# Performance work log

Measured on AMD Instinct MI355X. Metric: run time of the kernel, lower is better.

Reference implementation:

```python
import jax, jax.numpy as jnp
import numpy as np
from jax import lax

KS = 11          # kernel_size
SIGMA = 1.5
MAX_VAL = 1.0
C1 = (0.01 * MAX_VAL) ** 2
C2 = (0.03 * MAX_VAL) ** 2
EPS = 1e-12
PAD = KS // 2    # use_padding=True -> reflect pad


def _gaussian_kernel3d():
    ax = jnp.arange(KS, dtype=jnp.float32) - (KS - 1) / 2.0
    g = jnp.exp(-(ax[:, None, None] ** 2 + ax[None, :, None] ** 2 + ax[None, None, :] ** 2)
                / (2.0 * SIGMA ** 2))
    return g / g.sum()  # (KS, KS, KS)


def setup_inputs() -> dict:
    key = jax.random.key(0)
    k1, k2 = jax.random.split(key)
    shape = (2, 1, 160, 160, 160)
    source = jax.random.uniform(k1, shape, dtype=jnp.float32)
    reference_vol = jax.random.uniform(k2, shape, dtype=jnp.float32)
    return {"source": source, "reference": reference_vol}


def reference(source, reference):
    B, C, H, W, D = source.shape
    # reflect pad spatial dims (torch 'reflect' == numpy 'reflect')
    pad_cfg = ((0, 0), (0, 0), (PAD, PAD), (PAD, PAD), (PAD, PAD))
    src = jnp.pad(source, pad_cfg, mode="reflect")
    ref = jnp.pad(reference, pad_cfg, mode="reflect")

    # fuse the 5 depthwise convolutions into one grouped conv over stacked channels
    stacked = jnp.concatenate([src, ref, src * src, ref * ref, src * ref], axis=1)  # (B,5C,...)
    kern = _gaussian_kernel3d()[None, None]                      # (1,1,KS,KS,KS)
    kern = jnp.tile(kern, (5 * C, 1, 1, 1, 1))                   # (5C,1,KS,KS,KS)
    out = lax.conv_general_dilated(
        stacked, kern, window_strides=(1, 1, 1), padding="VALID",
        feature_group_count=5 * C,
        dimension_numbers=("NCDHW", "OIDHW", "NCDHW"))           # (B,5C,H,W,D)

    mu1 = out[:, 0 * C:1 * C]
    mu2 = out[:, 1 * C:2 * C]
    m11 = out[:, 2 * C:3 * C]
    m22 = out[:, 3 * C:4 * C]
    m12 = out[:, 4 * C:5 * C]

    mu1_sq = mu1 * mu1
    mu2_sq = mu2 * mu2
    mu1_mu2 = mu1 * mu2
    sigma1_sq = m11 - mu1_sq
    sigma2_sq = m22 - mu2_sq
    sigma12 = m12 - mu1_mu2

    numerator = (2.0 * mu1_mu2 + C1) * (2.0 * sigma12 + C2)
    denominator = (mu1_sq + mu2_sq + C1) * (sigma1_sq + sigma2_sq + C2)
    ssim = numerator / (denominator + EPS)
    return 1.0 - ssim.mean()
```

## Files before the change

### kernel.cpp

```cpp
#include <hip/hip_runtime.h>
#include <math.h>

#define HH 160
#define WW 160
#define DD 160
#define VOL (HH*WW*DD)
#define KS 11
#define PAD 5
#define NBATCH 2
#define NTOT (NBATCH*VOL)

#define WT 16
#define DT 16
#define HT 32
#define WPN (WT + 2*PAD)
#define NSTEP (HT + 2*PAD)
#define RS 68
#define P01S 36
#define P4S 17

typedef float v2f __attribute__((ext_vector_type(2)));
typedef float v4f __attribute__((ext_vector_type(4)));

struct Wts { float w[KS]; };

__device__ __forceinline__ int mirror(int i, int n) {
    if (i < 0) i = -i;
    if (i >= n) i = 2*n - 2 - i;
    return i;
}

__device__ __forceinline__ v2f pk_fma(v2f a, v2f b, v2f c) {
    v2f d;
    asm("v_pk_fma_f32 %0, %1, %2, %3" : "=v"(d) : "v"(a), "v"(b), "v"(c));
    return d;
}
__device__ __forceinline__ v2f pk_mul(v2f a, v2f b) {
    v2f d;
    asm("v_pk_mul_f32 %0, %1, %2" : "=v"(d) : "v"(a), "v"(b));
    return d;
}

__global__ void init_out(float* out) {
    if (threadIdx.x == 0 && blockIdx.x == 0) out[0] = 1.0f;
}

__global__ __launch_bounds__(256) void fused(const float* __restrict__ src,
                                             const float* __restrict__ ref,
                                             float* __restrict__ out,
                                             Wts wts, float scale) {
    __shared__ float raw[WPN * RS];
    __shared__ float pl01[WPN * P01S];
    __shared__ float pl23[WPN * P01S];
    __shared__ float pl4 [WPN * P4S];

    const int bx  = blockIdx.x;
    const int dt_ = bx % (DD/DT);
    const int wt_ = (bx / (DD/DT)) % (WW/WT);
    const int ht_ = (bx / ((DD/DT)*(WW/WT))) % (HH/HT);
    const int b   = bx / ((DD/DT)*(WW/WT)*(HH/HT));
    const int d0 = dt_*DT, w0 = wt_*WT, h0 = ht_*HT;

    const int  dbase = (d0 == 0) ? 0 : ((d0 == DD-DT) ? DD-32 : d0-8);
    const bool dedge = (d0 == 0) || (d0 == DD-DT);

    const int tid = threadIdx.x;
    const float* __restrict__ sp = src + (size_t)b*VOL;
    const float* __restrict__ rp = ref + (size_t)b*VOL;

    const bool sact = (tid < WPN*8);
    const int  swp = tid >> 3, sq = tid & 7;
    const int  sgoff  = mirror(w0 - PAD + (sact ? swp : 0), WW)*DD + dbase + sq*4;
    const int  srawof = swp*RS + sq*8;

    const int  p_dl  = tid & 15;
    const int  p_wp0 = tid >> 4;
    const bool p_act1 = (tid < WPN*DT - 256);
    const int  pw0_01 = p_wp0*P01S + 2*p_dl;
    const int  pw0_4  = p_wp0*P4S  + p_dl;
    const int  pw1_01 = (p_wp0+16)*P01S + 2*p_dl;
    const int  pw1_4  = (p_wp0+16)*P4S  + p_dl;

    const int wl = tid >> 4, dl2 = tid & 15;

    v2f wpk[KS];
#pragma unroll
    for (int k = 0; k < KS; ++k) { wpk[k].x = wts.w[k]; wpk[k].y = wts.w[k]; }

    v2f acc01[KS], acc23[KS];
    float acc4[KS];
#pragma unroll
    for (int s = 0; s < KS; ++s) {
        acc01[s] = (v2f)0.f; acc23[s] = (v2f)0.f; acc4[s] = 0.f;
    }

    float ssum = 0.f;

    v4f ra = (v4f)0.f, rb_ = (v4f)0.f;
    {
        const int hm = mirror(h0 - PAD, HH);
        if (sact) {
            const float* g = sp + (size_t)hm*(WW*DD) + sgoff;
            const float* h = rp + (size_t)hm*(WW*DD) + sgoff;
            ra  = *reinterpret_cast<const v4f*>(g);
            rb_ = *reinterpret_cast<const v4f*>(h);
        }
    }

    for (int tb = 0; tb < 44; tb += 11) {
#pragma unroll
        for (int ts = 0; ts < 11; ++ts) {
            const int t = tb + ts;
            if (t < NSTEP) {
                if (sact) {
                    v4f c0, c1;
                    c0.x = ra.x; c0.y = rb_.x; c0.z = ra.y; c0.w = rb_.y;
                    c1.x = ra.z; c1.y = rb_.z; c1.z = ra.w; c1.w = rb_.w;
                    *reinterpret_cast<v4f*>(&raw[srawof])     = c0;
                    *reinterpret_cast<v4f*>(&raw[srawof + 4]) = c1;
                }
                __syncthreads();

                {
                    v2f mu_a = (v2f)0.f, mm_a = (v2f)0.f;
                    v2f mu_b = (v2f)0.f, mm_b = (v2f)0.f;
                    float m12a = 0.f, m12b = 0.f;
                    if (!dedge) {
                        const float* r0 = &raw[p_wp0*RS + 2*(p_dl + 3)];
                        const float* r1 = r0 + 16*RS;
#pragma unroll
                        for (int k = 0; k < KS; ++k) {
                            v2f w  = wpk[k];
                            v2f sr = *reinterpret_cast<const v2f*>(r0 + 2*k);
                            mu_a = pk_fma(sr, w, mu_a);
                            mm_a = pk_fma(pk_mul(sr, sr), w, mm_a);
                            m12a = fmaf(w.x, sr.x*sr.y, m12a);
                        }
                        if (p_act1) {
#pragma unroll
                            for (int k = 0; k < KS; ++k) {
                                v2f w  = wpk[k];
                                v2f sr = *reinterpret_cast<const v2f*>(r1 + 2*k);
                                mu_b = pk_fma(sr, w, mu_b);
                                mm_b = pk_fma(pk_mul(sr, sr), w, mm_b);
                                m12b = fmaf(w.x, sr.x*sr.y, m12b);
                            }
                        }
                    } else {
#pragma unroll
                        for (int k = 0; k < KS; ++k) {
                            const int widx = mirror(d0 + p_dl - PAD + k, DD) - dbase;
                            v2f w  = wpk[k];
                            v2f sr = *reinterpret_cast<const v2f*>(&raw[p_wp0*RS + 2*widx]);
                            mu_a = pk_fma(sr, w, mu_a);
                            mm_a = pk_fma(pk_mul(sr, sr), w, mm_a);
                            m12a = fmaf(w.x, sr.x*sr.y, m12a);
                            if (p_act1) {
                                v2f sr2 = *reinterpret_cast<const v2f*>(&raw[(p_wp0+16)*RS + 2*widx]);
                                mu_b = pk_fma(sr2, w, mu_b);
                                mm_b = pk_fma(pk_mul(sr2, sr2), w, mm_b);
                                m12b = fmaf(w.x, sr2.x*sr2.y, m12b);
                            }
                        }
                    }
                    *reinterpret_cast<v2f*>(&pl01[pw0_01]) = mu_a;
                    *reinterpret_cast<v2f*>(&pl23[pw0_01]) = mm_a;
                    pl4[pw0_4] = m12a;
                    if (p_act1) {
                        *reinterpret_cast<v2f*>(&pl01[pw1_01]) = mu_b;
                        *reinterpret_cast<v2f*>(&pl23[pw1_01]) = mm_b;
                        pl4[pw1_4] = m12b;
                    }
                }

                {
                    const int tn = t + 1;
                    if (sact && tn < NSTEP) {
                        const int hm = mirror(h0 - PAD + tn, HH);
                        const float* g = sp + (size_t)hm*(WW*DD) + sgoff;
                        const float* h = rp + (size_t)hm*(WW*DD) + sgoff;
                        ra  = *reinterpret_cast<const v4f*>(g);
                        rb_ = *reinterpret_cast<const v4f*>(h);
                    }
                }
                __syncthreads();

                {
                    v2f v01 = (v2f)0.f, v23 = (v2f)0.f;
                    float v4v = 0.f;
                    const float* q01 = &pl01[wl*P01S + 2*dl2];
                    const float* q23 = &pl23[wl*P01S + 2*dl2];
                    const float* q4  = &pl4 [wl*P4S  + dl2];
#pragma unroll
                    for (int k = 0; k < KS; ++k) {
                        v2f w = wpk[k];
                        v01 = pk_fma(*reinterpret_cast<const v2f*>(q01 + k*P01S), w, v01);
                        v23 = pk_fma(*reinterpret_cast<const v2f*>(q23 + k*P01S), w, v23);
                        v4v = fmaf(w.x, q4[k*P4S], v4v);
                    }
#pragma unroll
                    for (int m = 0; m < 11; ++m) {
                        const int slot = (ts + m) % 11;
                        v2f wt = wpk[10 - m];
                        acc01[slot] = pk_fma(v01, wt, acc01[slot]);
                        acc23[slot] = pk_fma(v23, wt, acc23[slot]);
                        acc4[slot]  = fmaf(wt.x, v4v, acc4[slot]);
                    }
                    if (t >= 10) {
                        float mu1 = acc01[ts].x, mu2 = acc01[ts].y;
                        float m11 = acc23[ts].x, m22 = acc23[ts].y, m12 = acc4[ts];
                        float mu1sq = mu1*mu1, mu2sq = mu2*mu2, mu12 = mu1*mu2;
                        float s1 = m11 - mu1sq, s2 = m22 - mu2sq, s12 = m12 - mu12;
                        const float C1 = 1e-4f, C2 = 9e-4f;
                        float num = (2.f*mu12 + C1) * (2.f*s12 + C2);
                        float den = (mu1sq + mu2sq + C1) * (s1 + s2 + C2);
                        ssum += num / (den + 1e-12f);
                    }
                    acc01[ts] = (v2f)0.f; acc23[ts] = (v2f)0.f; acc4[ts] = 0.f;
                }
            }
        }
    }

#pragma unroll
    for (int off = 32; off > 0; off >>= 1)
        ssum += __shfl_down(ssum, off, 64);
    __shared__ float lsum[4];
    int lane = tid & 63, wid = tid >> 6;
    if (lane == 0) lsum[wid] = ssum;
    __syncthreads();
    if (tid == 0)
        atomicAdd(out, -(lsum[0]+lsum[1]+lsum[2]+lsum[3]) * scale);
}

extern "C" void kernel_launch(void* const* d_in, const int* in_sizes, int n_in,
                              void* d_out, int out_size, void* d_ws, size_t ws_size,
                              hipStream_t stream) {
    const float* src = (const float*)d_in[0];
    const float* ref = (const float*)d_in[1];
    float* out = (float*)d_out;

    Wts wts;
    {
        double g[KS], s = 0.0;
        for (int i = 0; i < KS; ++i) {
            double a = (double)i - (KS - 1) / 2.0;
            g[i] = exp(-(a * a) / (2.0 * 1.5 * 1.5));
            s += g[i];
        }
        for (int i = 0; i < KS; ++i) wts.w[i] = (float)(g[i] / s);
    }

    const float scale = 1.0f / (float)NTOT;

    init_out<<<1, 64, 0, stream>>>(out);
    const int g = NBATCH * (HH/HT) * (WW/WT) * (DD/DT);
    fused<<<g, 256, 0, stream>>>(src, ref, out, wts, scale);
}
```

Baseline: 213.0 us.

## Double-buffer LDS stages to drop a barrier and prefetch two rows ahead

Double-buffers the raw and pass-1 LDS arrays so each H-step needs one __syncthreads instead of two. Global loads are issued two rows ahead, and the raw tile is preloaded before the loop. The change also refactors the D-pass to compute w*x once and reuse it for the sum, square and cross terms. It precomputes the mirrored edge offsets, replaces the division with rcp plus one Newton step, and changes the P4S padding. The cost is doubled LDS use, which can lower occupancy, and possible bank conflicts from the changed P4S stride.

Result: no change. 212.5 us (-0.2%).

```diff
diff --git a/kernel.cpp b/kernel.cpp
--- a/kernel.cpp
+++ b/kernel.cpp
@@ -17,7 +17,10 @@
 #define NSTEP (HT + 2*PAD)
 #define RS 68
 #define P01S 36
-#define P4S 17
+#define P4S 16
+#define RAW_W (WPN*RS)
+#define P01_W (WPN*P01S)
+#define P4_W  (WPN*P4S)
 
 typedef float v2f __attribute__((ext_vector_type(2)));
 typedef float v4f __attribute__((ext_vector_type(4)));
@@ -31,14 +34,13 @@
 }
 
 __device__ __forceinline__ v2f pk_fma(v2f a, v2f b, v2f c) {
-    v2f d;
-    asm("v_pk_fma_f32 %0, %1, %2, %3" : "=v"(d) : "v"(a), "v"(b), "v"(c));
-    return d;
+    v2f d; asm("v_pk_fma_f32 %0, %1, %2, %3" : "=v"(d) : "v"(a), "v"(b), "v"(c)); return d;
 }
 __device__ __forceinline__ v2f pk_mul(v2f a, v2f b) {
-    v2f d;
-    asm("v_pk_mul_f32 %0, %1, %2" : "=v"(d) : "v"(a), "v"(b));
-    return d;
+    v2f d; asm("v_pk_mul_f32 %0, %1, %2" : "=v"(d) : "v"(a), "v"(b)); return d;
+}
+__device__ __forceinline__ v2f pk_add(v2f a, v2f b) {
+    v2f d; asm("v_pk_add_f32 %0, %1, %2" : "=v"(d) : "v"(a), "v"(b)); return d;
 }
 
 __global__ void init_out(float* out) {
@@ -49,10 +51,10 @@
                                              const float* __restrict__ ref,
                                              float* __restrict__ out,
                                              Wts wts, float scale) {
-    __shared__ float raw[WPN * RS];
-    __shared__ float pl01[WPN * P01S];
-    __shared__ float pl23[WPN * P01S];
-    __shared__ float pl4 [WPN * P4S];
+    __shared__ float raw [2*RAW_W];
+    __shared__ float pl01[2*P01_W];
+    __shared__ float pl23[2*P01_W];
+    __shared__ float pl4 [2*P4_W];
 
     const int bx  = blockIdx.x;
     const int dt_ = bx % (DD/DT);
@@ -81,6 +83,13 @@
     const int  pw1_01 = (p_wp0+16)*P01S + 2*p_dl;
     const int  pw1_4  = (p_wp0+16)*P4S  + p_dl;
 
+    int eoff[KS];
+    if (dedge) {
+#pragma unroll
+        for (int k = 0; k < KS; ++k)
+            eoff[k] = 2*(mirror(d0 + p_dl - PAD + k, DD) - dbase);
+    }
+
     const int wl = tid >> 4, dl2 = tid & 15;
 
     v2f wpk[KS];
@@ -94,18 +103,24 @@
         acc01[s] = (v2f)0.f; acc23[s] = (v2f)0.f; acc4[s] = 0.f;
     }
 
+    v4f ra = (v4f)0.f, rb_ = (v4f)0.f;
+    if (sact) {
+        const size_t o0 = (size_t)mirror(h0 - PAD, HH)*(WW*DD) + sgoff;
+        ra  = *reinterpret_cast<const v4f*>(sp + o0);
+        rb_ = *reinterpret_cast<const v4f*>(rp + o0);
+        v4f c0, c1;
+        c0.x=ra.x; c0.y=rb_.x; c0.z=ra.y; c0.w=rb_.y;
+        c1.x=ra.z; c1.y=rb_.z; c1.z=ra.w; c1.w=rb_.w;
+        *reinterpret_cast<v4f*>(&raw[srawof])     = c0;
+        *reinterpret_cast<v4f*>(&raw[srawof + 4]) = c1;
+        const size_t o1 = (size_t)mirror(h0 - PAD + 1, HH)*(WW*DD) + sgoff;
+        ra  = *reinterpret_cast<const v4f*>(sp + o1);
+        rb_ = *reinterpret_cast<const v4f*>(rp + o1);
+    }
+    __syncthreads();
+
     float ssum = 0.f;
-
-    v4f ra = (v4f)0.f, rb_ = (v4f)0.f;
-    {
-        const int hm = mirror(h0 - PAD, HH);
-        if (sact) {
-            const float* g = sp + (size_t)hm*(WW*DD) + sgoff;
-            const float* h = rp + (size_t)hm*(WW*DD) + sgoff;
-            ra  = *reinterpret_cast<const v4f*>(g);
-            rb_ = *reinterpret_cast<const v4f*>(h);
-        }
-    }
+    int rawRd = 0, rawWr = RAW_W, po01 = 0, po4 = 0;
 
     for (int tb = 0; tb < 44; tb += 11) {
 #pragma unroll
@@ -114,83 +129,74 @@
             if (t < NSTEP) {
                 if (sact) {
                     v4f c0, c1;
-                    c0.x = ra.x; c0.y = rb_.x; c0.z = ra.y; c0.w = rb_.y;
-                    c1.x = ra.z; c1.y = rb_.z; c1.z = ra.w; c1.w = rb_.w;
-                    *reinterpret_cast<v4f*>(&raw[srawof])     = c0;
-                    *reinterpret_cast<v4f*>(&raw[srawof + 4]) = c1;
-                }
-                __syncthreads();
-
-                {
-                    v2f mu_a = (v2f)0.f, mm_a = (v2f)0.f;
-                    v2f mu_b = (v2f)0.f, mm_b = (v2f)0.f;
-                    float m12a = 0.f, m12b = 0.f;
-                    if (!dedge) {
-                        const float* r0 = &raw[p_wp0*RS + 2*(p_dl + 3)];
-                        const float* r1 = r0 + 16*RS;
+                    c0.x=ra.x; c0.y=rb_.x; c0.z=ra.y; c0.w=rb_.y;
+                    c1.x=ra.z; c1.y=rb_.z; c1.z=ra.w; c1.w=rb_.w;
+                    *reinterpret_cast<v4f*>(&raw[rawWr + srawof])     = c0;
+                    *reinterpret_cast<v4f*>(&raw[rawWr + srawof + 4]) = c1;
+                    const size_t on = (size_t)mirror(h0 - PAD + t + 2, HH)*(WW*DD) + sgoff;
+                    ra  = *reinterpret_cast<const v4f*>(sp + on);
+                    rb_ = *reinterpret_cast<const v4f*>(rp + on);
+                }
+
+                v2f mu_a=(v2f)0.f, mm_a=(v2f)0.f, mu_b=(v2f)0.f, mm_b=(v2f)0.f;
+                float m12a=0.f, m12b=0.f;
+                if (!dedge) {
+                    const float* r0 = &raw[rawRd + p_wp0*RS + 2*p_dl + 6];
+                    const float* r1 = r0 + 16*RS;
+#pragma unroll
+                    for (int k = 0; k < KS; ++k) {
+                        v2f sr = *reinterpret_cast<const v2f*>(r0 + 2*k);
+                        v2f p  = pk_mul(sr, wpk[k]);
+                        mu_a = pk_add(mu_a, p);
+                        mm_a = pk_fma(p, sr, mm_a);
+                        m12a = fmaf(p.x, sr.y, m12a);
+                    }
+                    if (p_act1) {
 #pragma unroll
                         for (int k = 0; k < KS; ++k) {
-                            v2f w  = wpk[k];
-                            v2f sr = *reinterpret_cast<const v2f*>(r0 + 2*k);
-                            mu_a = pk_fma(sr, w, mu_a);
-                            mm_a = pk_fma(pk_mul(sr, sr), w, mm_a);
-                            m12a = fmaf(w.x, sr.x*sr.y, m12a);
+                            v2f sr = *reinterpret_cast<const v2f*>(r1 + 2*k);
+                            v2f p  = pk_mul(sr, wpk[k]);
+                            mu_b = pk_add(mu_b, p);
+                            mm_b = pk_fma(p, sr, mm_b);
+                            m12b = fmaf(p.x, sr.y, m12b);
                         }
+                    }
+                } else {
+                    const float* rb0 = &raw[rawRd + p_wp0*RS];
+                    const float* rb1 = rb0 + 16*RS;
+#pragma unroll
+                    for (int k = 0; k < KS; ++k) {
+                        v2f sr = *reinterpret_cast<const v2f*>(rb0 + eoff[k]);
+                        v2f p  = pk_mul(sr, wpk[k]);
+                        mu_a = pk_add(mu_a, p);
+                        mm_a = pk_fma(p, sr, mm_a);
+                        m12a = fmaf(p.x, sr.y, m12a);
                         if (p_act1) {
-#pragma unroll
-                            for (int k = 0; k < KS; ++k) {
-                                v2f w  = wpk[k];
-                                v2f sr = *reinterpret_cast<const v2f*>(r1 + 2*k);
-                                mu_b = pk_fma(sr, w, mu_b);
-                                mm_b = pk_fma(pk_mul(sr, sr), w, mm_b);
-                                m12b = fmaf(w.x, sr.x*sr.y, m12b);
-                            }
+                            v2f sr2 = *reinterpret_cast<const v2f*>(rb1 + eoff[k]);
+                            v2f p2  = pk_mul(sr2, wpk[k]);
+                            mu_b = pk_add(mu_b, p2);
+                            mm_b = pk_fma(p2, sr2, mm_b);
+                            m12b = fmaf(p2.x, sr2.y, m12b);
                         }
-                    } else {
-#pragma unroll
-                        for (int k = 0; k < KS; ++k) {
-                            const int widx = mirror(d0 + p_dl - PAD + k, DD) - dbase;
-                            v2f w  = wpk[k];
-                            v2f sr = *reinterpret_cast<const v2f*>(&raw[p_wp0*RS + 2*widx]);
-                            mu_a = pk_fma(sr, w, mu_a);
-                            mm_a = pk_fma(pk_mul(sr, sr), w, mm_a);
-                            m12a = fmaf(w.x, sr.x*sr.y, m12a);
-                            if (p_act1) {
-                                v2f sr2 = *reinterpret_cast<const v2f*>(&raw[(p_wp0+16)*RS + 2*widx]);
-                                mu_b = pk_fma(sr2, w, mu_b);
-                                mm_b = pk_fma(pk_mul(sr2, sr2), w, mm_b);
-                                m12b = fmaf(w.x, sr2.x*sr2.y, m12b);
-                            }
-                        }
-                    }
-                    *reinterpret_cast<v2f*>(&pl01[pw0_01]) = mu_a;
-                    *reinterpret_cast<v2f*>(&pl23[pw0_01]) = mm_a;
-                    pl4[pw0_4] = m12a;
-                    if (p_act1) {
-                        *reinterpret_cast<v2f*>(&pl01[pw1_01]) = mu_b;
-                        *reinterpret_cast<v2f*>(&pl23[pw1_01]) = mm_b;
-                        pl4[pw1_4] = m12b;
-                    }
-                }
-
-                {
-                    const int tn = t + 1;
-                    if (sact && tn < NSTEP) {
-                        const int hm = mirror(h0 - PAD + tn, HH);
-                        const float* g = sp + (size_t)hm*(WW*DD) + sgoff;
-                        const float* h = rp + (size_t)hm*(WW*DD) + sgoff;
-                        ra  = *reinterpret_cast<const v4f*>(g);
-                        rb_ = *reinterpret_cast<const v4f*>(h);
-                    }
-                }
+                    }
+                }
+                *reinterpret_cast<v2f*>(&pl01[po01 + pw0_01]) = mu_a;
+                *reinterpret_cast<v2f*>(&pl23[po01 + pw0_01]) = mm_a;
+                pl4[po4 + pw0_4] = m12a;
+                if (p_act1) {
+                    *reinterpret_cast<v2f*>(&pl01[po01 + pw1_01]) = mu_b;
+                    *reinterpret_cast<v2f*>(&pl23[po01 + pw1_01]) = mm_b;
+                    pl4[po4 + pw1_4] = m12b;
+                }
+
                 __syncthreads();
 
                 {
                     v2f v01 = (v2f)0.f, v23 = (v2f)0.f;
                     float v4v = 0.f;
-                    const float* q01 = &pl01[wl*P01S + 2*dl2];
-                    const float* q23 = &pl23[wl*P01S + 2*dl2];
-                    const float* q4  = &pl4 [wl*P4S  + dl2];
+                    const float* q01 = &pl01[po01 + wl*P01S + 2*dl2];
+                    const float* q23 = &pl23[po01 + wl*P01S + 2*dl2];
+                    const float* q4  = &pl4 [po4  + wl*P4S  + dl2];
 #pragma unroll
                     for (int k = 0; k < KS; ++k) {
                         v2f w = wpk[k];
@@ -213,11 +219,15 @@
                         float s1 = m11 - mu1sq, s2 = m22 - mu2sq, s12 = m12 - mu12;
                         const float C1 = 1e-4f, C2 = 9e-4f;
                         float num = (2.f*mu12 + C1) * (2.f*s12 + C2);
-                        float den = (mu1sq + mu2sq + C1) * (s1 + s2 + C2);
-                        ssum += num / (den + 1e-12f);
+                        float den = (mu1sq + mu2sq + C1) * (s1 + s2 + C2) + 1e-12f;
+                        float inv = __builtin_amdgcn_rcpf(den);
+                        inv = inv * (2.0f - den * inv);
+                        ssum = fmaf(num, inv, ssum);
                     }
                     acc01[ts] = (v2f)0.f; acc23[ts] = (v2f)0.f; acc4[ts] = 0.f;
                 }
+
+                rawRd ^= RAW_W; rawWr ^= RAW_W; po01 ^= P01_W; po4 ^= P4_W;
             }
         }
     }
```
